# Optimization experiments

Hardware: AMD Instinct MI355X
Metric: run time of the kernel (lower is better)

## Reference

```python
import jax, jax.numpy as jnp
import numpy as np

M_MOL = 8192      # number of molecules
A_ATOMS = 32      # atoms per molecule (uniform ragged groups)
N_FEAT = 128      # schnet n_atom_basis


def setup_inputs() -> dict:
    key = jax.random.key(0)
    sr = jax.random.normal(key, (M_MOL * A_ATOMS, N_FEAT), dtype=jnp.float32)
    # idx_m: sorted molecule index per atom, uniform group sizes
    idx_m = jnp.repeat(jnp.arange(M_MOL, dtype=jnp.int32), A_ATOMS)
    return {"scalar_representation": sr, "idx_m": idx_m}


def reference(scalar_representation, idx_m):
    # maxm = int(idx_m[-1]) + 1 in the torch code; groups are uniform here so
    # torch.split over bincount == a simple reshape into [M, A, F].
    maxm = int(idx_m[-1]) + 1
    n_atoms = scalar_representation.shape[0]
    a = n_atoms // maxm
    sr = scalar_representation.reshape(maxm, a, -1)          # [M, A, F]
    # per-molecule correlation (Gram) matrix: c = sr @ sr.T
    c = jnp.einsum('maf,mbf->mab', sr, sr)                    # [M, A, A]
    # eigvalsh returns ascending eigenvalues; torch code takes [0] (smallest)
    eigvals = jnp.linalg.eigvalsh(c)                          # [M, A]
    return eigvals[:, 0]                                      # [M]
```

## Files before the change

kernel.cpp:

```cpp
#include <hip/hip_runtime.h>
#include <hip/hip_bf16.h>

#define DEVINL __device__ __forceinline__

typedef __attribute__((ext_vector_type(8))) short short8;
typedef __attribute__((ext_vector_type(4))) float f32x4;

DEVINL float rcp_f(float x) { return __builtin_amdgcn_rcpf(x); }

#define LDS_FENCE() __asm__ volatile("" ::: "memory")

template<int CTRL>
DEVINL float dpp_mov(float x) {
  return __int_as_float(__builtin_amdgcn_update_dpp(
      0, __float_as_int(x), CTRL, 0xF, 0xF, true));
}
DEVINL float pair_sum(float x) { return x + dpp_mov<0xB1>(x); }

DEVINL short bf_hi(float f, float& rem) {
  unsigned u = __float_as_uint(f);
  unsigned rh = (u + 0x8000u) >> 16;
  rem = f - __uint_as_float(rh << 16);
  return (short)rh;
}
DEVINL short bf_of(float f) {
  return (short)((__float_as_uint(f) + 0x8000u) >> 16);
}
DEVINL void cvt_hilo(float4 fa, float4 fb, short8& h, short8& lo) {
  float rm;
  h[0] = bf_hi(fa.x, rm); lo[0] = bf_of(rm);
  h[1] = bf_hi(fa.y, rm); lo[1] = bf_of(rm);
  h[2] = bf_hi(fa.z, rm); lo[2] = bf_of(rm);
  h[3] = bf_hi(fa.w, rm); lo[3] = bf_of(rm);
  h[4] = bf_hi(fb.x, rm); lo[4] = bf_of(rm);
  h[5] = bf_hi(fb.y, rm); lo[5] = bf_of(rm);
  h[6] = bf_hi(fb.z, rm); lo[6] = bf_of(rm);
  h[7] = bf_hi(fb.w, rm); lo[7] = bf_of(rm);
}
DEVINL f32x4 mfma_bf16(short8 a, short8 b, f32x4 c) {
  return __builtin_amdgcn_mfma_f32_16x16x32_bf16(a, b, c, 0, 0, 0);
}

template<int K>
DEVINL void house_step(float (&r)[16], int row, int h,
                       float* vbuf, float* pbuf, float* de) {
  constexpr int HK = K >> 4, EK = K & 15;
  constexpr int HP = (K + 1) >> 4, PE = (K + 1) & 15;
  constexpr int PC = PE >> 2, PEE = PE & 3;

  float xm = (row > K) ? r[EK] : 0.0f;
  if (h == HK) vbuf[row] = xm;
  LDS_FENCE();

  float4 vc[4];
  #pragma unroll
  for (int j = 0; j < 4; ++j) vc[j] = *(const float4*)(vbuf + 16 * h + 4 * j);
  float x_me = vbuf[row];
  float x0   = vbuf[K + 1];

  float n0 = 0.f, n1 = 0.f;
  #pragma unroll
  for (int j = 0; j < 4; ++j) {
    n0 = fmaf(vc[j].x, vc[j].x, n0); n1 = fmaf(vc[j].y, vc[j].y, n1);
    n0 = fmaf(vc[j].z, vc[j].z, n0); n1 = fmaf(vc[j].w, vc[j].w, n1);
  }
  float nn = pair_sum(n0 + n1);

  float alpha = -copysignf(sqrtf(nn), x0);
  float denom = nn - alpha * x0;
  float beta  = (denom > 1e-20f) ? rcp_f(denom) : 0.0f;
  float v_me  = x_me - ((row == K + 1) ? alpha : 0.0f);

  if (h == HP) {
    if constexpr (PEE == 0)      vc[PC].x -= alpha;
    else if constexpr (PEE == 1) vc[PC].y -= alpha;
    else if constexpr (PEE == 2) vc[PC].z -= alpha;
    else                         vc[PC].w -= alpha;
  }

  float a0 = 0.f, a1 = 0.f;
  #pragma unroll
  for (int j = 0; j < 4; ++j) {
    a0 = fmaf(r[4 * j + 0], vc[j].x, a0); a1 = fmaf(r[4 * j + 1], vc[j].y, a1);
    a0 = fmaf(r[4 * j + 2], vc[j].z, a0); a1 = fmaf(r[4 * j + 3], vc[j].w, a1);
  }
  float p_me = pair_sum(a0 + a1);
  if (h == 0) pbuf[row] = p_me;
  LDS_FENCE();

  float bv = beta * v_me;
  float bp = (row > K) ? beta * p_me : 0.0f;

  float g0 = 0.f, g1 = 0.f;
  #pragma unroll
  for (int j = 0; j < 4; ++j) {
    float4 pcx = *(const float4*)(pbuf + 16 * h + 4 * j);
    g0 = fmaf(vc[j].x, pcx.x, g0); g1 = fmaf(vc[j].y, pcx.y, g1);
    g0 = fmaf(vc[j].z, pcx.z, g0); g1 = fmaf(vc[j].w, pcx.w, g1);
    r[4 * j + 0] -= bv * pcx.x + bp * vc[j].x;
    r[4 * j + 1] -= bv * pcx.y + bp * vc[j].y;
    r[4 * j + 2] -= bv * pcx.z + bp * vc[j].z;
    r[4 * j + 3] -= bv * pcx.w + bp * vc[j].w;
  }
  float G  = pair_sum(g0 + g1);
  float tv = (beta * beta * G) * v_me;

  #pragma unroll
  for (int j = 0; j < 4; ++j) {
    r[4 * j + 0] = fmaf(tv, vc[j].x, r[4 * j + 0]);
    r[4 * j + 1] = fmaf(tv, vc[j].y, r[4 * j + 1]);
    r[4 * j + 2] = fmaf(tv, vc[j].z, r[4 * j + 2]);
    r[4 * j + 3] = fmaf(tv, vc[j].w, r[4 * j + 3]);
  }

  if (row == K && h == HK) { de[K] = r[EK]; de[32 + K] = alpha; }
}

template<int K>
DEVINL void house_all(float (&r)[16], int row, int h,
                      float* vbuf, float* pbuf, float* de) {
  house_step<K>(r, row, h, vbuf, pbuf, de);
  if constexpr (K < 30) house_all<K + 1>(r, row, h, vbuf, pbuf, de);
}

__global__ __launch_bounds__(256) void Correlation_85134841741354_kernel(
    const float* __restrict__ A, float* __restrict__ out, int M) {
  const int lane = threadIdx.x & 63;
  const int wave = threadIdx.x >> 6;
  const int q    = lane >> 4;
  const int t    = lane & 15;
  const int row  = lane >> 1;
  const int h    = lane & 1;
  const int mol  = blockIdx.x * 4 + wave;
  if (mol >= M) return;

  __shared__ float ldsT[4][32 * 36 + 8];
  float* tq = &ldsT[wave][0];

  {
    const float* Am = A + (size_t)mol * (32 * 128);
    f32x4 acc00 = {0.f, 0.f, 0.f, 0.f}, acc01 = {0.f, 0.f, 0.f, 0.f};
    f32x4 acc10 = {0.f, 0.f, 0.f, 0.f}, acc11 = {0.f, 0.f, 0.f, 0.f};
    #pragma unroll
    for (int c = 0; c < 4; ++c) {
      const float* pr0 = Am + t * 128        + 32 * c + 8 * q;
      const float* pr1 = Am + (t + 16) * 128 + 32 * c + 8 * q;
      float4 fa0 = *(const float4*)(pr0);
      float4 fb0 = *(const float4*)(pr0 + 4);
      float4 fa1 = *(const float4*)(pr1);
      float4 fb1 = *(const float4*)(pr1 + 4);
      short8 h0, l0, h1, l1;
      cvt_hilo(fa0, fb0, h0, l0);
      cvt_hilo(fa1, fb1, h1, l1);
      acc00 = mfma_bf16(h0, h0, acc00); acc00 = mfma_bf16(h0, l0, acc00); acc00 = mfma_bf16(l0, h0, acc00);
      acc01 = mfma_bf16(h0, h1, acc01); acc01 = mfma_bf16(h0, l1, acc01); acc01 = mfma_bf16(l0, h1, acc01);
      acc10 = mfma_bf16(h1, h0, acc10); acc10 = mfma_bf16(h1, l0, acc10); acc10 = mfma_bf16(l1, h0, acc10);
      acc11 = mfma_bf16(h1, h1, acc11); acc11 = mfma_bf16(h1, l1, acc11); acc11 = mfma_bf16(l1, h1, acc11);
    }
    #pragma unroll
    for (int reg = 0; reg < 4; ++reg) {
      tq[(4 * q + reg) * 36 + t]           = acc00[reg];
      tq[(4 * q + reg) * 36 + 16 + t]      = acc01[reg];
      tq[(16 + 4 * q + reg) * 36 + t]      = acc10[reg];
      tq[(16 + 4 * q + reg) * 36 + 16 + t] = acc11[reg];
    }
  }
  LDS_FENCE();

  float r[16];
  #pragma unroll
  for (int j = 0; j < 4; ++j) {
    float4 x = *(const float4*)(tq + row * 36 + 16 * h + 4 * j);
    r[4 * j + 0] = x.x; r[4 * j + 1] = x.y;
    r[4 * j + 2] = x.z; r[4 * j + 3] = x.w;
  }
  LDS_FENCE();

  float* vbuf = tq;
  float* pbuf = tq + 40;
  float* de   = tq + 80;

  house_all<0>(r, row, h, vbuf, pbuf, de);
  if (row == 31 && h == 1) { de[31] = r[15]; de[63] = 0.0f; }
  LDS_FENCE();

  float vd[32], ve[32];
  #pragma unroll
  for (int c = 0; c < 8; ++c) {
    float4 dc = *(const float4*)(de + 4 * c);
    float4 ec = *(const float4*)(de + 32 + 4 * c);
    vd[4 * c + 0] = dc.x; vd[4 * c + 1] = dc.y;
    vd[4 * c + 2] = dc.z; vd[4 * c + 3] = dc.w;
    ve[4 * c + 0] = ec.x; ve[4 * c + 1] = ec.y;
    ve[4 * c + 2] = ec.z; ve[4 * c + 3] = ec.w;
  }
  float glo = vd[0] - fabsf(ve[0]);
  float ghi = vd[0] + fabsf(ve[0]);
  #pragma unroll
  for (int i = 1; i < 32; ++i) {
    float rad = fabsf(ve[i]) + fabsf(ve[i - 1]);
    glo = fminf(glo, vd[i] - rad);
    ghi = fmaxf(ghi, vd[i] + rad);
  }
  float lo = fmaxf(glo - 1e-3f, 0.0f);
  float hi = ghi + 1e-3f;

  #pragma unroll
  for (int i = 0; i < 32; ++i) ve[i] *= ve[i];

  #pragma unroll
  for (int rr = 0; rr < 3; ++rr) {
    float stp = (hi - lo) * (1.0f / 65.0f);
    float sig = fmaf(stp, (float)(lane + 1), lo);
    float qq = vd[0] - sig;
    int cnt = (qq < 0.0f) ? 1 : 0;
    #pragma unroll
    for (int i = 1; i < 32; ++i) {
      float qs = (fabsf(qq) < 1e-12f) ? ((qq < 0.0f) ? -1e-12f : 1e-12f) : qq;
      qq = (vd[i] - sig) - ve[i - 1] * rcp_f(qs);
      cnt += (qq < 0.0f) ? 1 : 0;
    }
    unsigned long long m64 = __ballot(cnt >= 1);
    int b = (m64 == 0ull) ? 64 : (__ffsll((unsigned long long)m64) - 1);
    float nhi = (b == 64) ? hi : fmaf(stp, (float)(b + 1), lo);
    lo = fmaf(stp, (float)b, lo);
    hi = nhi;
  }

  if (lane == 0) out[mol] = 0.5f * (lo + hi);
}

extern "C" void kernel_launch(void* const* d_in, const int* in_sizes, int n_in,
                              void* d_out, int out_size, void* d_ws, size_t ws_size,
                              hipStream_t stream) {
  const float* A = (const float*)d_in[0];
  float* out = (float*)d_out;
  int n_atoms = in_sizes[1];
  int M = n_atoms / 32;
  int blocks = (M + 3) / 4;
  hipLaunchKernelGGL(Correlation_85134841741354_kernel,
                     dim3(blocks), dim3(256), 0, stream, A, out, M);
}
```

Before: 228.3 us.

## Keep full matrix rows per lane and broadcast via readlane instead of LDS

Result: slower. 242.4 us (+6.2%).

```diff
diff --git a/kernel.cpp b/kernel.cpp
--- a/kernel.cpp
+++ b/kernel.cpp
@@ -15,7 +15,22 @@
   return __int_as_float(__builtin_amdgcn_update_dpp(
       0, __float_as_int(x), CTRL, 0xF, 0xF, true));
 }
-DEVINL float pair_sum(float x) { return x + dpp_mov<0xB1>(x); }
+DEVINL float readlane_f(float v, int lane) {
+  return __int_as_float(__builtin_amdgcn_readlane(__float_as_int(v), lane));
+}
+DEVINL float readfirst_f(float v) {
+  return __int_as_float(__builtin_amdgcn_readfirstlane(__float_as_int(v)));
+}
+
+constexpr int lane_of_row(int m) { return (m & 15) + 32 * (m >> 4); }
+
+DEVINL float sum_rows(float x) {
+  x += dpp_mov<0xB1>(x);
+  x += dpp_mov<0x4E>(x);
+  x += dpp_mov<0x141>(x);
+  x += dpp_mov<0x140>(x);
+  return readlane_f(x, 0) + readlane_f(x, 32);
+}
 
 DEVINL short bf_hi(float f, float& rem) {
   unsigned u = __float_as_uint(f);
@@ -42,85 +57,57 @@
 }
 
 template<int K>
-DEVINL void house_step(float (&r)[16], int row, int h,
-                       float* vbuf, float* pbuf, float* de) {
-  constexpr int HK = K >> 4, EK = K & 15;
-  constexpr int HP = (K + 1) >> 4, PE = (K + 1) & 15;
-  constexpr int PC = PE >> 2, PEE = PE & 3;
-
-  float xm = (row > K) ? r[EK] : 0.0f;
-  if (h == HK) vbuf[row] = xm;
-  LDS_FENCE();
-
-  float4 vc[4];
-  #pragma unroll
-  for (int j = 0; j < 4; ++j) vc[j] = *(const float4*)(vbuf + 16 * h + 4 * j);
-  float x_me = vbuf[row];
-  float x0   = vbuf[K + 1];
-
-  float n0 = 0.f, n1 = 0.f;
-  #pragma unroll
-  for (int j = 0; j < 4; ++j) {
-    n0 = fmaf(vc[j].x, vc[j].x, n0); n1 = fmaf(vc[j].y, vc[j].y, n1);
-    n0 = fmaf(vc[j].z, vc[j].z, n0); n1 = fmaf(vc[j].w, vc[j].w, n1);
-  }
-  float nn = pair_sum(n0 + n1);
-
+DEVINL void house_step(float (&r)[32], int row,
+                       float (&sd)[32], float (&se)[32]) {
+  float xm = (row > K) ? r[K] : 0.0f;
+
+  float sx[32];
+  #pragma unroll
+  for (int m = K + 1; m < 32; ++m) sx[m] = readlane_f(r[K], lane_of_row(m));
+
+  float nn = sum_rows(xm * xm);
+  float x0 = sx[K + 1];
   float alpha = -copysignf(sqrtf(nn), x0);
   float denom = nn - alpha * x0;
   float beta  = (denom > 1e-20f) ? rcp_f(denom) : 0.0f;
-  float v_me  = x_me - ((row == K + 1) ? alpha : 0.0f);
-
-  if (h == HP) {
-    if constexpr (PEE == 0)      vc[PC].x -= alpha;
-    else if constexpr (PEE == 1) vc[PC].y -= alpha;
-    else if constexpr (PEE == 2) vc[PC].z -= alpha;
-    else                         vc[PC].w -= alpha;
-  }
+  float v_me  = xm - ((row == K + 1) ? alpha : 0.0f);
+  float vpiv  = x0 - alpha;
 
   float a0 = 0.f, a1 = 0.f;
   #pragma unroll
-  for (int j = 0; j < 4; ++j) {
-    a0 = fmaf(r[4 * j + 0], vc[j].x, a0); a1 = fmaf(r[4 * j + 1], vc[j].y, a1);
-    a0 = fmaf(r[4 * j + 2], vc[j].z, a0); a1 = fmaf(r[4 * j + 3], vc[j].w, a1);
-  }
-  float p_me = pair_sum(a0 + a1);
-  if (h == 0) pbuf[row] = p_me;
-  LDS_FENCE();
+  for (int m = K + 1; m < 32; ++m) {
+    float vm = (m == K + 1) ? vpiv : sx[m];
+    if ((m - K) & 1) a1 = fmaf(r[m], vm, a1);
+    else             a0 = fmaf(r[m], vm, a0);
+  }
+  float p_me = a0 + a1;
+
+  float G = sum_rows(v_me * p_me);
+  float sp[32];
+  #pragma unroll
+  for (int m = K + 1; m < 32; ++m) sp[m] = readlane_f(p_me, lane_of_row(m));
 
   float bv = beta * v_me;
   float bp = (row > K) ? beta * p_me : 0.0f;
-
-  float g0 = 0.f, g1 = 0.f;
-  #pragma unroll
-  for (int j = 0; j < 4; ++j) {
-    float4 pcx = *(const float4*)(pbuf + 16 * h + 4 * j);
-    g0 = fmaf(vc[j].x, pcx.x, g0); g1 = fmaf(vc[j].y, pcx.y, g1);
-    g0 = fmaf(vc[j].z, pcx.z, g0); g1 = fmaf(vc[j].w, pcx.w, g1);
-    r[4 * j + 0] -= bv * pcx.x + bp * vc[j].x;
-    r[4 * j + 1] -= bv * pcx.y + bp * vc[j].y;
-    r[4 * j + 2] -= bv * pcx.z + bp * vc[j].z;
-    r[4 * j + 3] -= bv * pcx.w + bp * vc[j].w;
-  }
-  float G  = pair_sum(g0 + g1);
   float tv = (beta * beta * G) * v_me;
-
-  #pragma unroll
-  for (int j = 0; j < 4; ++j) {
-    r[4 * j + 0] = fmaf(tv, vc[j].x, r[4 * j + 0]);
-    r[4 * j + 1] = fmaf(tv, vc[j].y, r[4 * j + 1]);
-    r[4 * j + 2] = fmaf(tv, vc[j].z, r[4 * j + 2]);
-    r[4 * j + 3] = fmaf(tv, vc[j].w, r[4 * j + 3]);
-  }
-
-  if (row == K && h == HK) { de[K] = r[EK]; de[32 + K] = alpha; }
+  float nbv = -bv;
+  float nw  = tv - bp;
+
+  #pragma unroll
+  for (int m = K + 1; m < 32; ++m) {
+    float vm = (m == K + 1) ? vpiv : sx[m];
+    r[m] = fmaf(nbv, sp[m], fmaf(nw, vm, r[m]));
+  }
+
+  sd[K] = readlane_f(r[K], lane_of_row(K));
+  se[K] = readfirst_f(fabsf(alpha));
 }
 
 template<int K>
-DEVINL void house_all(float (&r)[16], int row, int h,
-                      float* vbuf, float* pbuf, float* de) {
-  house_step<K>(r, row, h, vbuf, pbuf, de);
-  if constexpr (K < 30) house_all<K + 1>(r, row, h, vbuf, pbuf, de);
+DEVINL void house_all(float (&r)[32], int row,
+                      float (&sd)[32], float (&se)[32]) {
+  house_step<K>(r, row, sd, se);
+  if constexpr (K < 30) house_all<K + 1>(r, row, sd, se);
 }
 
 __global__ __launch_bounds__(256) void Correlation_85134841741354_kernel(
@@ -129,8 +116,7 @@
   const int wave = threadIdx.x >> 6;
   const int q    = lane >> 4;
   const int t    = lane & 15;
-  const int row  = lane >> 1;
-  const int h    = lane & 1;
+  const int row  = (lane & 15) + 16 * (lane >> 5);
   const int mol  = blockIdx.x * 4 + wave;
   if (mol >= M) return;
 
@@ -167,57 +153,44 @@
   }
   LDS_FENCE();
 
-  float r[16];
-  #pragma unroll
-  for (int j = 0; j < 4; ++j) {
-    float4 x = *(const float4*)(tq + row * 36 + 16 * h + 4 * j);
-    r[4 * j + 0] = x.x; r[4 * j + 1] = x.y;
-    r[4 * j + 2] = x.z; r[4 * j + 3] = x.w;
-  }
-  LDS_FENCE();
-
-  float* vbuf = tq;
-  float* pbuf = tq + 40;
-  float* de   = tq + 80;
-
-  house_all<0>(r, row, h, vbuf, pbuf, de);
-  if (row == 31 && h == 1) { de[31] = r[15]; de[63] = 0.0f; }
-  LDS_FENCE();
-
-  float vd[32], ve[32];
+  float r[32];
   #pragma unroll
   for (int c = 0; c < 8; ++c) {
-    float4 dc = *(const float4*)(de + 4 * c);
-    float4 ec = *(const float4*)(de + 32 + 4 * c);
-    vd[4 * c + 0] = dc.x; vd[4 * c + 1] = dc.y;
-    vd[4 * c + 2] = dc.z; vd[4 * c + 3] = dc.w;
-    ve[4 * c + 0] = ec.x; ve[4 * c + 1] = ec.y;
-    ve[4 * c + 2] = ec.z; ve[4 * c + 3] = ec.w;
-  }
-  float glo = vd[0] - fabsf(ve[0]);
-  float ghi = vd[0] + fabsf(ve[0]);
+    float4 x = *(const float4*)(tq + row * 36 + 4 * c);
+    r[4 * c + 0] = x.x; r[4 * c + 1] = x.y;
+    r[4 * c + 2] = x.z; r[4 * c + 3] = x.w;
+  }
+
+  float sd[32], se[32];
+  house_all<0>(r, row, sd, se);
+  sd[31] = readlane_f(r[31], lane_of_row(31));
+  se[31] = 0.0f;
+
+  float glo = sd[0] - se[0];
+  float ghi = sd[0] + se[0];
   #pragma unroll
   for (int i = 1; i < 32; ++i) {
-    float rad = fabsf(ve[i]) + fabsf(ve[i - 1]);
-    glo = fminf(glo, vd[i] - rad);
-    ghi = fmaxf(ghi, vd[i] + rad);
+    float rad = se[i] + se[i - 1];
+    glo = fminf(glo, sd[i] - rad);
+    ghi = fmaxf(ghi, sd[i] + rad);
   }
   float lo = fmaxf(glo - 1e-3f, 0.0f);
   float hi = ghi + 1e-3f;
 
-  #pragma unroll
-  for (int i = 0; i < 32; ++i) ve[i] *= ve[i];
+  float se2[32];
+  #pragma unroll
+  for (int i = 0; i < 32; ++i) se2[i] = se[i] * se[i];
 
   #pragma unroll
   for (int rr = 0; rr < 3; ++rr) {
     float stp = (hi - lo) * (1.0f / 65.0f);
     float sig = fmaf(stp, (float)(lane + 1), lo);
-    float qq = vd[0] - sig;
+    float qq = sd[0] - sig;
     int cnt = (qq < 0.0f) ? 1 : 0;
     #pragma unroll
     for (int i = 1; i < 32; ++i) {
       float qs = (fabsf(qq) < 1e-12f) ? ((qq < 0.0f) ? -1e-12f : 1e-12f) : qq;
-      qq = (vd[i] - sig) - ve[i - 1] * rcp_f(qs);
+      qq = (sd[i] - sig) - se2[i - 1] * rcp_f(qs);
       cnt += (qq < 0.0f) ? 1 : 0;
     }
     unsigned long long m64 = __ballot(cnt >= 1);
```
